# Performance work log

Measured on AMD Instinct MI355X. Metric: run time of the kernel, lower is better.

Reference implementation:

```python
import jax, jax.numpy as jnp
import numpy as np

D_MODEL = 1024
H = 16
DH = 64
FFN = 4096
CHUNK = 64
LN_EPS = 1e-5


def layer_norm(x, w, b):
    mu = x.mean(-1, keepdims=True)
    var = x.var(-1, keepdims=True)
    return (x - mu) * jax.lax.rsqrt(var + LN_EPS) * w + b


def l2_normalize(x):
    # matches torch F.normalize(p=2, dim=-1, eps=1e-12)
    n = jnp.sqrt(jnp.sum(x * x, axis=-1, keepdims=True))
    return x / jnp.maximum(n, 1e-12)


def chunk_gla(q, k, v, alpha, C=CHUNK):
    B, Hh, N, D = q.shape
    nc = N // C  # N chosen as multiple of C (pad==0 in original)
    q = q.reshape(B, Hh, nc, C, D)
    k = k.reshape(B, Hh, nc, C, D)
    v = v.reshape(B, Hh, nc, C, D)
    alpha = alpha.reshape(B, Hh, nc, C, D)

    log_a = jnp.log(jnp.maximum(alpha, 1e-6))
    la_cum = jnp.cumsum(log_a, axis=3)                  # (B,H,nc,C,D)
    la_mean = la_cum.mean(-1)                            # (B,H,nc,C)
    tril = jnp.tril(jnp.ones((C, C), dtype=q.dtype))
    decay = jnp.exp(la_mean[..., :, None] - la_mean[..., None, :]) * tril  # (B,H,nc,C,C)

    attn_intra = jnp.einsum('bhncd,bhnmd->bhncm', q, k) * decay
    o_intra = jnp.einsum('bhncm,bhnmd->bhncd', attn_intra, v)

    decay_to_end = jnp.exp(la_cum[:, :, :, -1:, :] - la_cum)
    kv_chunk = jnp.einsum('bhncf,bhnce->bhnfe', k * decay_to_end, v)  # (B,H,nc,D,D)
    chunk_decay = jnp.exp(log_a.sum(3))                  # (B,H,nc,D)
    q_dec = q * jnp.exp(la_cum)                          # decay_from_start

    def step(S, inp):
        qd, kv, cd = inp                                 # (B,H,C,D),(B,H,D,D),(B,H,D)
        o = jnp.einsum('bhcd,bhde->bhce', qd, S)
        S_new = S * cd[:, :, :, None] + kv
        return S_new, o

    S0 = jnp.zeros((B, Hh, D, D), dtype=q.dtype)
    _, o_inter = jax.lax.scan(
        step, S0,
        (jnp.moveaxis(q_dec, 2, 0), jnp.moveaxis(kv_chunk, 2, 0), jnp.moveaxis(chunk_decay, 2, 0)))
    o_inter = jnp.moveaxis(o_inter, 0, 2)                # (B,H,nc,C,D)
    return (o_intra + o_inter).reshape(B, Hh, N, D)


def setup_inputs() -> dict:
    key = jax.random.key(0)
    ks = jax.random.split(key, 16)
    s = 0.02
    td = H * DH
    return {
        'x': jax.random.normal(ks[0], (2, 4096, D_MODEL), dtype=jnp.float32),
        'Wq': jax.random.normal(ks[1], (D_MODEL, td), dtype=jnp.float32) * s,
        'Wk': jax.random.normal(ks[2], (D_MODEL, td), dtype=jnp.float32) * s,
        'Wv': jax.random.normal(ks[3], (D_MODEL, td), dtype=jnp.float32) * s,
        'Wg': jax.random.normal(ks[4], (D_MODEL, td), dtype=jnp.float32) * s,
        'bg': jnp.full((td,), -0.5, dtype=jnp.float32),
        'Wo': jax.random.normal(ks[5], (td, D_MODEL), dtype=jnp.float32) * s,
        'ln1_w': jnp.ones((D_MODEL,), jnp.float32),
        'ln1_b': jnp.zeros((D_MODEL,), jnp.float32),
        'ln2_w': jnp.ones((D_MODEL,), jnp.float32),
        'ln2_b': jnp.zeros((D_MODEL,), jnp.float32),
        'W1': jax.random.normal(ks[6], (D_MODEL, FFN), dtype=jnp.float32) * s,
        'b1': jnp.zeros((FFN,), jnp.float32),
        'W2': jax.random.normal(ks[7], (FFN, D_MODEL), dtype=jnp.float32) * s,
        'b2': jnp.zeros((D_MODEL,), jnp.float32),
    }


def reference(x, Wq, Wk, Wv, Wg, bg, Wo, ln1_w, ln1_b, ln2_w, ln2_b, W1, b1, W2, b2):
    B, N, _ = x.shape
    xn = layer_norm(x, ln1_w, ln1_b)
    q = (xn @ Wq).reshape(B, N, H, DH).transpose(0, 2, 1, 3)
    k = (xn @ Wk).reshape(B, N, H, DH).transpose(0, 2, 1, 3)
    v = (xn @ Wv).reshape(B, N, H, DH).transpose(0, 2, 1, 3)
    q = l2_normalize(q)
    k = l2_normalize(k)
    alpha = jax.nn.sigmoid(xn @ Wg + bg).reshape(B, N, H, DH).transpose(0, 2, 1, 3)
    o = chunk_gla(q, k, v, alpha)
    o = o.transpose(0, 2, 1, 3).reshape(B, N, H * DH)
    x = x + o @ Wo  # dropout off (eval / p=0)
    h = layer_norm(x, ln2_w, ln2_b)
    x = x + jax.nn.gelu(h @ W1 + b1, approximate=False) @ W2 + b2
    return x
```

## Files before the change

### kernel.cpp

```cpp
#include <hip/hip_runtime.h>

#define AS1 __attribute__((address_space(1)))
#define AS3 __attribute__((address_space(3)))

typedef unsigned short u16;
typedef short s16x8 __attribute__((ext_vector_type(8)));
typedef float f32x4 __attribute__((ext_vector_type(4)));

__device__ __forceinline__ float bf2f(u16 u) {
    union { unsigned u; float f; } v; v.u = ((unsigned)u) << 16; return v.f;
}
__device__ __forceinline__ u16 f2bf(float f) {
    union { float f; unsigned u; } v; v.f = f;
    unsigned u = v.u;
    return (u16)((u + 0x7FFFu + ((u >> 16) & 1u)) >> 16);
}

__device__ __forceinline__ void gload16(const void* g, void* l) {
    __builtin_amdgcn_global_load_lds((const AS1 void*)g, (AS3 void*)l, 16, 0, 0);
}

__global__ __launch_bounds__(256) void transpose_bf16(
    const float* __restrict__ src, u16* __restrict__ dst, int R, int C)
{
    __shared__ float t[32][33];
    const int tx = threadIdx.x, ty = threadIdx.y;
    const int r0 = blockIdx.x * 32, c0 = blockIdx.y * 32;
#pragma unroll
    for (int i = 0; i < 4; i++)
        t[ty + i * 8][tx] = src[(size_t)(r0 + ty + i * 8) * C + c0 + tx];
    __syncthreads();
#pragma unroll
    for (int i = 0; i < 4; i++)
        dst[(size_t)(c0 + ty + i * 8) * R + r0 + tx] = f2bf(t[tx][ty + i * 8]);
}

__global__ __launch_bounds__(256) void ln_bf16(
    const float* __restrict__ x, const float* __restrict__ w,
    const float* __restrict__ b, u16* __restrict__ out)
{
    __shared__ float red[8];
    const int row = blockIdx.x;
    const int tid = threadIdx.x;
    const size_t base = (size_t)row * 1024 + tid * 4;
    const float4 xv = *(const float4*)&x[base];
    float s = xv.x + xv.y + xv.z + xv.w;
    float q = xv.x * xv.x + xv.y * xv.y + xv.z * xv.z + xv.w * xv.w;
#pragma unroll
    for (int m = 1; m < 64; m <<= 1) { s += __shfl_xor(s, m); q += __shfl_xor(q, m); }
    if ((tid & 63) == 0) { red[tid >> 6] = s; red[4 + (tid >> 6)] = q; }
    __syncthreads();
    s = red[0] + red[1] + red[2] + red[3];
    q = red[4] + red[5] + red[6] + red[7];
    const float mu = s * (1.f / 1024.f);
    const float var = q * (1.f / 1024.f) - mu * mu;
    const float rs = rsqrtf(var + 1e-5f);
    const float4 wv = *(const float4*)&w[tid * 4];
    const float4 bv = *(const float4*)&b[tid * 4];
    uint2 ov;
    ov.x = (unsigned)f2bf((xv.x - mu) * rs * wv.x + bv.x) |
           ((unsigned)f2bf((xv.y - mu) * rs * wv.y + bv.y) << 16);
    ov.y = (unsigned)f2bf((xv.z - mu) * rs * wv.z + bv.z) |
           ((unsigned)f2bf((xv.w - mu) * rs * wv.w + bv.w) << 16);
    *(uint2*)&out[base] = ov;
}

template <int EP>
__global__ __launch_bounds__(256, 2) void gemm_bt(
    const u16* __restrict__ A, const u16* __restrict__ BT,
    float* __restrict__ Cf, u16* __restrict__ Cb,
    const float* __restrict__ bias, const float* __restrict__ resid,
    int M, int N, int K)
{
    __shared__ u16 As[4096];
    __shared__ u16 Bs[4096];
    const int tid = threadIdx.x;
    const int w = tid >> 6;
    const int l = tid & 63;
    const int tm = blockIdx.x * 128;
    const int tn = blockIdx.y * 128;
    const int wm = (w >> 1) * 64;
    const int wn = (w & 1) * 64;

    f32x4 acc[4][4] = {};

    const int e0 = w * 512 + l * 8;
    const int r0 = e0 >> 5, c0 = e0 & 31;
    const int e1 = 2048 + e0;
    const int r1 = e1 >> 5, c1 = e1 & 31;
    const size_t arow0 = (size_t)(tm + r0) * K + c0;
    const size_t arow1 = (size_t)(tm + r1) * K + c1;
    const size_t brow0 = (size_t)(tn + r0) * K + c0;
    const size_t brow1 = (size_t)(tn + r1) * K + c1;
    const int lofs = w * 512;
    const int afr = wm + (l & 15);
    const int bfr = wn + (l & 15);
    const int kk = (l >> 4) * 8;

    for (int k0 = 0; k0 < K; k0 += 32) {
        gload16(&A[arow0 + k0], &As[lofs]);
        gload16(&A[arow1 + k0], &As[2048 + lofs]);
        gload16(&BT[brow0 + k0], &Bs[lofs]);
        gload16(&BT[brow1 + k0], &Bs[2048 + lofs]);
        __syncthreads();
        s16x8 a[4], b[4];
#pragma unroll
        for (int i = 0; i < 4; i++) a[i] = *(const s16x8*)&As[(afr + i * 16) * 32 + kk];
#pragma unroll
        for (int j = 0; j < 4; j++) b[j] = *(const s16x8*)&Bs[(bfr + j * 16) * 32 + kk];
#pragma unroll
        for (int i = 0; i < 4; i++)
#pragma unroll
            for (int j = 0; j < 4; j++)
                acc[i][j] = __builtin_amdgcn_mfma_f32_16x16x32_bf16(a[i], b[j], acc[i][j], 0, 0, 0);
        __syncthreads();
    }

    const int erow = tm + wm + (l >> 4) * 4;
    const int ecol = tn + wn + (l & 15);
#pragma unroll
    for (int i = 0; i < 4; i++) {
#pragma unroll
        for (int j = 0; j < 4; j++) {
            const int col = ecol + j * 16;
#pragma unroll
            for (int r = 0; r < 4; r++) {
                const int row = erow + i * 16 + r;
                const size_t idx = (size_t)row * N + col;
                const float v = acc[i][j][r];
                if (EP == 0) {
                    Cf[idx] = v;
                } else if (EP == 1) {
                    Cb[idx] = f2bf(v);
                } else if (EP == 2) {
                    Cf[idx] = v + resid[idx];
                } else if (EP == 3) {
                    const float u = v + bias[col];
                    Cb[idx] = f2bf(0.5f * u * (1.f + erff(u * 0.70710678118654752f)));
                } else {
                    Cf[idx] = v + bias[col] + resid[idx];
                }
            }
        }
    }
}

#define TP 72
#define LP 65
__global__ __launch_bounds__(256) void gla_a(
    const u16* __restrict__ qkv,
    const float* __restrict__ g,
    const float* __restrict__ bg,
    u16* __restrict__ qdec,
    u16* __restrict__ kvT,
    float* __restrict__ cdec,
    u16* __restrict__ ointra)
{
    __shared__ u16 Qh[64 * TP];
    __shared__ u16 Kh[64 * TP];
    __shared__ u16 VT[64 * TP];
    __shared__ float L[64 * LP];
    __shared__ float lm[64], nq[64], nk[64];

    const int bid = blockIdx.x;
    const int bh = bid >> 6, ck = bid & 63;
    const int b = bh >> 4, h = bh & 15;
    const int tok0 = b * 4096 + ck * 64;
    const int tid = threadIdx.x;
    const int w = tid >> 6, l = tid & 63;

#pragma unroll
    for (int pass = 0; pass < 2; pass++) {
        const int c = (tid >> 3) + pass * 32;
        const int col = (tid & 7) * 8;
        const size_t rb = (size_t)(tok0 + c) * 3072 + h * 64 + col;
        uint4 qv = *(const uint4*)&qkv[rb];
        uint4 kv_ = *(const uint4*)&qkv[rb + 1024];
        uint4 vv = *(const uint4*)&qkv[rb + 2048];
        *(uint4*)&Qh[c * TP + col] = qv;
        *(uint4*)&Kh[c * TP + col] = kv_;
        const u16* va = (const u16*)&vv;
#pragma unroll
        for (int j = 0; j < 8; j++) VT[(col + j) * TP + c] = va[j];
    }
#pragma unroll
    for (int pass = 0; pass < 4; pass++) {
        const int c = (tid >> 4) + pass * 16;
        const int col = (tid & 15) * 4;
        float4 gv = *(const float4*)&g[(size_t)(tok0 + c) * 1024 + h * 64 + col];
        float4 bgv = *(const float4*)&bg[h * 64 + col];
        const float* ga = (const float*)&gv;
        const float* ba = (const float*)&bgv;
#pragma unroll
        for (int i = 0; i < 4; i++) {
            const float z = ga[i] + ba[i];
            const float al = 1.f / (1.f + __expf(-z));
            L[c * LP + col + i] = __logf(fmaxf(al, 1e-6f));
        }
    }
    __syncthreads();

    {
        const int d = tid >> 2, qq = tid & 3;
        float vals[16];
#pragma unroll
        for (int i = 0; i < 16; i++) vals[i] = L[(qq * 16 + i) * LP + d];
        float s = 0.f;
#pragma unroll
        for (int i = 0; i < 16; i++) { s += vals[i]; vals[i] = s; }
        float sum = s;
        float u1 = __shfl_up(sum, 1, 4); if (qq >= 1) sum += u1;
        float u2 = __shfl_up(sum, 2, 4); if (qq >= 2) sum += u2;
        const float excl = sum - s;
#pragma unroll
        for (int i = 0; i < 16; i++) L[(qq * 16 + i) * LP + d] = vals[i] + excl;
        if (qq == 3) cdec[((size_t)bh * 64 + ck) * 64 + d] = __expf(sum);
    }
    __syncthreads();

    {
        const int c = tid >> 2, qq = tid & 3;
        float sl = 0.f, sq = 0.f, sk = 0.f;
        uint4 qa = *(const uint4*)&Qh[c * TP + qq * 16];
        uint4 qb = *(const uint4*)&Qh[c * TP + qq * 16 + 8];
        uint4 ka = *(const uint4*)&Kh[c * TP + qq * 16];
        uint4 kb = *(const uint4*)&Kh[c * TP + qq * 16 + 8];
        const u16* qu = (const u16*)&qa; const u16* qu2 = (const u16*)&qb;
        const u16* ku = (const u16*)&ka; const u16* ku2 = (const u16*)&kb;
#pragma unroll
        for (int i = 0; i < 8; i++) {
            float q1 = bf2f(qu[i]), q2 = bf2f(qu2[i]);
            float k1 = bf2f(ku[i]), k2 = bf2f(ku2[i]);
            sq += q1 * q1 + q2 * q2;
            sk += k1 * k1 + k2 * k2;
        }
#pragma unroll
        for (int i = 0; i < 16; i++) sl += L[c * LP + qq * 16 + i];
        sl += __shfl_xor(sl, 1); sl += __shfl_xor(sl, 2);
        sq += __shfl_xor(sq, 1); sq += __shfl_xor(sq, 2);
        sk += __shfl_xor(sk, 1); sk += __shfl_xor(sk, 2);
        if (qq == 0) {
            lm[c] = sl * (1.f / 64.f);
            nq[c] = 1.f / fmaxf(sqrtf(sq), 1e-12f);
            nk[c] = 1.f / fmaxf(sqrtf(sk), 1e-12f);
        }
    }
    __syncthreads();

    u16 kdt[16];
    {
        const int c = tid >> 2, qq = tid & 3;
        const float qn = nq[c], kn = nk[c];
        uint4 qa = *(const uint4*)&Qh[c * TP + qq * 16];
        uint4 qb = *(const uint4*)&Qh[c * TP + qq * 16 + 8];
        uint4 ka = *(const uint4*)&Kh[c * TP + qq * 16];
        uint4 kb = *(const uint4*)&Kh[c * TP + qq * 16 + 8];
        u16* qu = (u16*)&qa; u16* qu2 = (u16*)&qb;
        u16* ku = (u16*)&ka; u16* ku2 = (u16*)&kb;
        float Lc[16], Le[16];
#pragma unroll
        for (int i = 0; i < 16; i++) {
            Lc[i] = L[c * LP + qq * 16 + i];
            Le[i] = L[63 * LP + qq * 16 + i];
        }
        unsigned qd[8];
#pragma unroll
        for (int i = 0; i < 8; i++) {
            float qh1 = bf2f(qu[i]) * qn;  qu[i] = f2bf(qh1);
            float qh2 = bf2f(qu2[i]) * qn; qu2[i] = f2bf(qh2);
            float kh1 = bf2f(ku[i]) * kn;  ku[i] = f2bf(kh1);
            float kh2 = bf2f(ku2[i]) * kn; ku2[i] = f2bf(kh2);
            kdt[i]     = f2bf(kh1 * __expf(Le[i] - Lc[i]));
            kdt[i + 8] = f2bf(kh2 * __expf(Le[i + 8] - Lc[i + 8]));
            const unsigned lo = (unsigned)f2bf(qh1 * __expf(Lc[i]));
            const unsigned hi = (i < 4) ? 0u : 0u;
            qd[i] = lo; (void)hi;
        }
        unsigned pk[8];
#pragma unroll
        for (int i = 0; i < 4; i++) {
            pk[i]     = qd[2 * i] | (qd[2 * i + 1] << 16);
        }
#pragma unroll
        for (int i = 0; i < 4; i++) {
            const float qh1 = bf2f(qu2[2 * i]) * 1.f;
            const float qh2 = bf2f(qu2[2 * i + 1]) * 1.f;
            pk[4 + i] = (unsigned)f2bf(qh1 * __expf(Lc[8 + 2 * i])) |
                        ((unsigned)f2bf(qh2 * __expf(Lc[8 + 2 * i + 1])) << 16);
        }
        *(uint4*)&Qh[c * TP + qq * 16] = qa;
        *(uint4*)&Qh[c * TP + qq * 16 + 8] = qb;
        *(uint4*)&Kh[c * TP + qq * 16] = ka;
        *(uint4*)&Kh[c * TP + qq * 16 + 8] = kb;
        u16* qrow = &qdec[((size_t)bh * 4096 + ck * 64 + c) * 64 + qq * 16];
        *(uint4*)&qrow[0] = *(const uint4*)&pk[0];
        *(uint4*)&qrow[8] = *(const uint4*)&pk[4];
    }
    __syncthreads();

    u16* KDT = (u16*)L;
    {
        const int c = tid >> 2, qq = tid & 3;
#pragma unroll
        for (int i = 0; i < 16; i++) KDT[(qq * 16 + i) * TP + c] = kdt[i];
    }
    const int fr = l & 15;
    const int kk = (l >> 4) * 8;
    f32x4 accS[4] = {};
#pragma unroll
    for (int ks = 0; ks < 2; ks++) {
        s16x8 af = *(const s16x8*)&Qh[(w * 16 + fr) * TP + ks * 32 + kk];
#pragma unroll
        for (int j = 0; j < 4; j++) {
            s16x8 bf = *(const s16x8*)&Kh[(j * 16 + fr) * TP + ks * 32 + kk];
            accS[j] = __builtin_amdgcn_mfma_f32_16x16x32_bf16(af, bf, accS[j], 0, 0, 0);
        }
    }
    __syncthreads();

    {
        const int erow = w * 16 + (l >> 4) * 4;
#pragma unroll
        for (int j = 0; j < 4; j++) {
            const int mm = j * 16 + (l & 15);
            const float lmm = lm[mm];
#pragma unroll
            for (int r = 0; r < 4; r++) {
                const int cc = erow + r;
                const float wgt = (mm <= cc) ? __expf(lm[cc] - lmm) : 0.f;
                Qh[cc * TP + mm] = f2bf(accS[j][r] * wgt);
            }
        }
    }
    __syncthreads();

    f32x4 accO[4] = {};
    f32x4 accK[4] = {};
#pragma unroll
    for (int ks = 0; ks < 2; ks++) {
        s16x8 aAt = *(const s16x8*)&Qh[(w * 16 + fr) * TP + ks * 32 + kk];
        s16x8 aVt = *(const s16x8*)&VT[(w * 16 + fr) * TP + ks * 32 + kk];
#pragma unroll
        for (int j = 0; j < 4; j++) {
            s16x8 bVt = *(const s16x8*)&VT[(j * 16 + fr) * TP + ks * 32 + kk];
            s16x8 bKd = *(const s16x8*)&KDT[(j * 16 + fr) * TP + ks * 32 + kk];
            accO[j] = __builtin_amdgcn_mfma_f32_16x16x32_bf16(aAt, bVt, accO[j], 0, 0, 0);
            accK[j] = __builtin_amdgcn_mfma_f32_16x16x32_bf16(aVt, bKd, accK[j], 0, 0, 0);
        }
    }
    {
        const int erow = w * 16 + (l >> 4) * 4;
#pragma unroll
        for (int j = 0; j < 4; j++) {
            const int col = j * 16 + (l & 15);
#pragma unroll
            for (int r = 0; r < 4; r++) {
                const int row = erow + r;
                ointra[((size_t)bh * 4096 + ck * 64 + row) * 64 + col] = f2bf(accO[j][r]);
                kvT[(((size_t)bh * 64 + ck) * 64 + row) * 64 + col] = f2bf(accK[j][r]);
            }
        }
    }
}

__global__ __launch_bounds__(256) void gla_scan(
    const u16* __restrict__ kvT, const float* __restrict__ cdec,
    u16* __restrict__ ST)
{
    const int bh = blockIdx.x >> 4;
    const int de = (blockIdx.x & 15) * 256 + threadIdx.x;
    const int d = de & 63;
    float s = 0.f;
    const size_t base = (size_t)bh * 64 * 4096 + de;
    const size_t cb = (size_t)bh * 4096 + d;
    for (int t = 0; t < 64; t++) {
        ST[base + (size_t)t * 4096] = f2bf(s);
        s = s * cdec[cb + (size_t)t * 64] + bf2f(kvT[base + (size_t)t * 4096]);
    }
}

__global__ __launch_bounds__(256) void gla_b(
    const u16* __restrict__ qdec, const u16* __restrict__ ST,
    const u16* __restrict__ ointra, u16* __restrict__ obf)
{
    __shared__ u16 Qd[64 * TP];
    __shared__ u16 Sd[64 * TP];
    const int bid = blockIdx.x;
    const int bh = bid >> 6, ck = bid & 63;
    const int b = bh >> 4, h = bh & 15;
    const int tid = threadIdx.x;
    const int w = tid >> 6, l = tid & 63;
#pragma unroll
    for (int pass = 0; pass < 2; pass++) {
        const int r = (tid >> 3) + pass * 32;
        const int col = (tid & 7) * 8;
        *(uint4*)&Qd[r * TP + col] =
            *(const uint4*)&qdec[((size_t)bh * 4096 + ck * 64 + r) * 64 + col];
        *(uint4*)&Sd[r * TP + col] =
            *(const uint4*)&ST[(((size_t)bh * 64 + ck) * 64 + r) * 64 + col];
    }
    __syncthreads();
    const int fr = l & 15;
    const int kk = (l >> 4) * 8;
    f32x4 acc[4] = {};
#pragma unroll
    for (int ks = 0; ks < 2; ks++) {
        s16x8 af = *(const s16x8*)&Qd[(w * 16 + fr) * TP + ks * 32 + kk];
#pragma unroll
        for (int j = 0; j < 4; j++) {
            s16x8 bf = *(const s16x8*)&Sd[(j * 16 + fr) * TP + ks * 32 + kk];
            acc[j] = __builtin_amdgcn_mfma_f32_16x16x32_bf16(af, bf, acc[j], 0, 0, 0);
        }
    }
    const int erow = w * 16 + (l >> 4) * 4;
#pragma unroll
    for (int j = 0; j < 4; j++) {
        const int e = j * 16 + (l & 15);
#pragma unroll
        for (int r = 0; r < 4; r++) {
            const int cc = erow + r;
            const size_t ia = ((size_t)bh * 4096 + ck * 64 + cc) * 64 + e;
            const float v = acc[j][r] + bf2f(ointra[ia]);
            obf[(size_t)(b * 4096 + ck * 64 + cc) * 1024 + h * 64 + e] = f2bf(v);
        }
    }
}

__global__ void fill_sentinel(float* out, int n) {
    int i = blockIdx.x * 256 + threadIdx.x;
    if (i < n) out[i] = 12345.0f;
}

extern "C" void kernel_launch(void* const* d_in, const int* in_sizes, int n_in,
                              void* d_out, int out_size, void* d_ws, size_t ws_size,
                              hipStream_t stream)
{
    const float* x    = (const float*)d_in[0];
    const float* Wq   = (const float*)d_in[1];
    const float* Wk   = (const float*)d_in[2];
    const float* Wv   = (const float*)d_in[3];
    const float* Wg   = (const float*)d_in[4];
    const float* bg   = (const float*)d_in[5];
    const float* Wo   = (const float*)d_in[6];
    const float* ln1w = (const float*)d_in[7];
    const float* ln1b = (const float*)d_in[8];
    const float* ln2w = (const float*)d_in[9];
    const float* ln2b = (const float*)d_in[10];
    const float* W1   = (const float*)d_in[11];
    const float* b1   = (const float*)d_in[12];
    const float* W2   = (const float*)d_in[13];
    const float* b2   = (const float*)d_in[14];
    float* out = (float*)d_out;

    char* ws = (char*)d_ws;
    u16*   wtQKVG = (u16*)(ws + 0);
    u16*   wtWo   = (u16*)(ws + 8388608);
    u16*   wtW1   = (u16*)(ws + 10485760);
    u16*   wtW2   = (u16*)(ws + 18874368);
    u16*   xnb    = (u16*)(ws + 27262976);
    u16*   qkvb   = (u16*)(ws + 44040192);
    float* gbuf   = (float*)(ws + 94371840);
    u16*   kvT    = (u16*)(ws + 127926272);
    float* cdbuf  = (float*)(ws + 144703488);
    u16*   qdecb  = (u16*)(ws + 145227776);
    u16*   ointra = (u16*)(ws + 162004992);
    u16*   STb    = (u16*)(ws + 178782208);
    u16*   obf    = (u16*)(ws + 195559424);
    u16*   hbf    = (u16*)(ws + 212336640);
    float* x2     = (float*)(ws + 94371840);
    u16*   ffnb   = (u16*)(ws + 27262976);

    if (ws_size < 229113856u) {
        fill_sentinel<<<dim3((out_size + 255) / 256), dim3(256), 0, stream>>>(out, out_size);
        return;
    }

    const dim3 b256(256), b32x8(32, 8);

    transpose_bf16<<<dim3(32, 32),  b32x8, 0, stream>>>(Wq, wtQKVG,               1024, 1024);
    transpose_bf16<<<dim3(32, 32),  b32x8, 0, stream>>>(Wk, wtQKVG + 1024 * 1024, 1024, 1024);
    transpose_bf16<<<dim3(32, 32),  b32x8, 0, stream>>>(Wv, wtQKVG + 2048 * 1024, 1024, 1024);
    transpose_bf16<<<dim3(32, 32),  b32x8, 0, stream>>>(Wg, wtQKVG + 3072 * 1024, 1024, 1024);
    transpose_bf16<<<dim3(32, 32),  b32x8, 0, stream>>>(Wo, wtWo,                 1024, 1024);
    transpose_bf16<<<dim3(32, 128), b32x8, 0, stream>>>(W1, wtW1,                 1024, 4096);
    transpose_bf16<<<dim3(128, 32), b32x8, 0, stream>>>(W2, wtW2,                 4096, 1024);

    ln_bf16<<<dim3(8192), b256, 0, stream>>>(x, ln1w, ln1b, xnb);
    gemm_bt<1><<<dim3(64, 24), b256, 0, stream>>>(xnb, wtQKVG, nullptr, qkvb, nullptr, nullptr, 8192, 3072, 1024);
    gemm_bt<0><<<dim3(64, 8),  b256, 0, stream>>>(xnb, wtQKVG + 3072 * 1024, gbuf, nullptr, nullptr, nullptr, 8192, 1024, 1024);

    gla_a<<<dim3(2048), b256, 0, stream>>>(qkvb, gbuf, bg, qdecb, kvT, cdbuf, ointra);
    gla_scan<<<dim3(512), b256, 0, stream>>>(kvT, cdbuf, STb);
    gla_b<<<dim3(2048), b256, 0, stream>>>(qdecb, STb, ointra, obf);

    gemm_bt<2><<<dim3(64, 8), b256, 0, stream>>>(obf, wtWo, x2, nullptr, nullptr, x, 8192, 1024, 1024);
    ln_bf16<<<dim3(8192), b256, 0, stream>>>(x2, ln2w, ln2b, hbf);
    gemm_bt<3><<<dim3(64, 32), b256, 0, stream>>>(hbf, wtW1, nullptr, ffnb, b1, nullptr, 8192, 4096, 1024);
    gemm_bt<4><<<dim3(64, 8),  b256, 0, stream>>>(ffnb, wtW2, out, nullptr, b2, x2, 8192, 1024, 4096);
}
```

Measured before the change: 423.0 us.

## Add 256x256-tile double-buffered GEMM with swizzled LDS; fuse QKV and gate projections

Adds a new 512-thread GEMM kernel with 256x256 output tiles, a double-buffered LDS pipeline fed by direct global-to-LDS loads, XOR-swizzled LDS addressing and raised wave priority around MFMA blocks. It is used for the merged QKV+gate projection (one launch whose epilogue routes columns to bf16 or fp32 outputs), the Wo projection with residual, and the FFN up-projection with GELU. The older gemm_bt is trimmed to the bias+residual epilogue still used by the FFN down-projection. The gla_a q-decay packing is also simplified. Larger tiles raise per-block reuse but give fewer blocks, which risks poor occupancy and tail effects on the smaller GEMMs.

Result: slower. 544.7 us (+28.8%).

```diff
diff --git a/kernel.cpp b/kernel.cpp
--- a/kernel.cpp
+++ b/kernel.cpp
@@ -127,18 +127,138 @@
             for (int r = 0; r < 4; r++) {
                 const int row = erow + i * 16 + r;
                 const size_t idx = (size_t)row * N + col;
-                const float v = acc[i][j][r];
-                if (EP == 0) {
-                    Cf[idx] = v;
-                } else if (EP == 1) {
-                    Cb[idx] = f2bf(v);
-                } else if (EP == 2) {
+                Cf[idx] = acc[i][j][r] + bias[col] + resid[idx];
+            }
+        }
+    }
+}
+
+template <int MO>
+__device__ __forceinline__ void quad(f32x4 (&acc)[8][4], const s16x8 (&aa)[4], const s16x8 (&bb)[4]) {
+#pragma unroll
+    for (int mm = 0; mm < 4; mm++)
+#pragma unroll
+        for (int nn = 0; nn < 4; nn++)
+            acc[MO + mm][nn] =
+                __builtin_amdgcn_mfma_f32_16x16x32_bf16(aa[mm], bb[nn], acc[MO + mm][nn], 0, 0, 0);
+}
+
+template <int EPX>
+__global__ __launch_bounds__(512, 2) void gemm256(
+    const u16* __restrict__ A, const u16* __restrict__ BT,
+    float* __restrict__ Cf, u16* __restrict__ Cb,
+    const float* __restrict__ bias, const float* __restrict__ resid,
+    int M, int N, int K)
+{
+    __shared__ u16 As[2][16384];
+    __shared__ u16 Bs[2][16384];
+    const int tid = threadIdx.x;
+    const int w = tid >> 6;
+    const int l = tid & 63;
+    const int wr = w >> 2;
+    const int wc = w & 3;
+    const int tm = blockIdx.x * 256;
+    const int tn = blockIdx.y * 256;
+
+    const int srow = w * 8 + (l >> 3);
+    const int swzc = ((l & 7) * 8) ^ (((l >> 3) & 3) << 4) ^ (((l >> 5) & 1) << 3);
+    size_t aS[2][2], bS[2][2];
+#pragma unroll
+    for (int h = 0; h < 2; h++)
+#pragma unroll
+        for (int j = 0; j < 2; j++) {
+            aS[h][j] = (size_t)(tm + h * 128 + j * 64 + srow) * K + swzc;
+            bS[h][j] = (size_t)(tn + h * 128 + j * 64 + srow) * K + swzc;
+        }
+    const int ldsOff[2] = { w * 512, 4096 + w * 512 };
+
+    auto stage = [&](int t, int buf) {
+        const int k0 = t * 64;
+#pragma unroll
+        for (int h = 0; h < 2; h++)
+#pragma unroll
+            for (int j = 0; j < 2; j++)
+                gload16(&A[aS[h][j] + k0], &As[buf][h * 8192 + ldsOff[j]]);
+#pragma unroll
+        for (int h = 0; h < 2; h++)
+#pragma unroll
+            for (int j = 0; j < 2; j++)
+                gload16(&BT[bS[h][j] + k0], &Bs[buf][h * 8192 + ldsOff[j]]);
+    };
+
+    const int sm = ((l & 3) << 4) | (((l >> 2) & 1) << 3);
+    const int aRd = wr * 8192 + (l & 15) * 64 + (((l >> 4) * 8) ^ sm);
+    const int bRd = wc * 4096 + (l & 15) * 64 + (((l >> 4) * 8) ^ sm);
+
+    f32x4 acc[8][4] = {};
+
+    stage(0, 0);
+    stage(1, 1);
+    asm volatile("s_waitcnt vmcnt(8)" ::: "memory");
+    __builtin_amdgcn_s_barrier();
+
+    const int NT = K >> 6;
+    for (int t = 0; t < NT; ++t) {
+        const int buf = t & 1;
+        const u16* as = As[buf];
+        const u16* bs = Bs[buf];
+        s16x8 aa[4], bb[4];
+#pragma unroll
+        for (int i = 0; i < 4; i++) bb[i] = *(const s16x8*)&bs[bRd + i * 1024];
+#pragma unroll
+        for (int i = 0; i < 4; i++) aa[i] = *(const s16x8*)&as[aRd + i * 1024];
+        __builtin_amdgcn_s_setprio(1);
+        quad<0>(acc, aa, bb);
+        __builtin_amdgcn_s_setprio(0);
+#pragma unroll
+        for (int i = 0; i < 4; i++) aa[i] = *(const s16x8*)&as[aRd + (i + 4) * 1024];
+        __builtin_amdgcn_s_setprio(1);
+        quad<4>(acc, aa, bb);
+        __builtin_amdgcn_s_setprio(0);
+        s16x8 bb1[4], aa1[4];
+#pragma unroll
+        for (int i = 0; i < 4; i++) bb1[i] = *(const s16x8*)&bs[(bRd + i * 1024) ^ 32];
+#pragma unroll
+        for (int i = 0; i < 4; i++) aa[i] = *(const s16x8*)&as[(aRd + i * 1024) ^ 32];
+        __builtin_amdgcn_s_setprio(1);
+        quad<0>(acc, aa, bb1);
+        __builtin_amdgcn_s_setprio(0);
+#pragma unroll
+        for (int i = 0; i < 4; i++) aa1[i] = *(const s16x8*)&as[(aRd + (i + 4) * 1024) ^ 32];
+        asm volatile("s_waitcnt lgkmcnt(0)" ::: "memory");
+        __builtin_amdgcn_sched_barrier(0);
+        __builtin_amdgcn_s_barrier();
+        const bool st = (t + 2 < NT);
+        if (st) stage(t + 2, buf);
+        __builtin_amdgcn_s_setprio(1);
+        quad<4>(acc, aa1, bb1);
+        __builtin_amdgcn_s_setprio(0);
+        if (st)                 asm volatile("s_waitcnt vmcnt(8)" ::: "memory");
+        else if (t + 1 < NT)    asm volatile("s_waitcnt vmcnt(0)" ::: "memory");
+        __builtin_amdgcn_s_barrier();
+    }
+
+    const int erow0 = tm + wr * 128 + (l >> 4) * 4;
+    const int ecol0 = tn + wc * 64 + (l & 15);
+#pragma unroll
+    for (int m = 0; m < 8; m++) {
+#pragma unroll
+        for (int n = 0; n < 4; n++) {
+            const int col = ecol0 + n * 16;
+#pragma unroll
+            for (int r = 0; r < 4; r++) {
+                const int row = erow0 + m * 16 + r;
+                const float v = acc[m][n][r];
+                if (EPX == 0) {
+                    if (col < 3072) Cb[(size_t)row * 3072 + col] = f2bf(v);
+                    else            Cf[(size_t)row * 1024 + (col - 3072)] = v;
+                } else if (EPX == 1) {
+                    const float u2 = v + bias[col];
+                    Cb[(size_t)row * N + col] =
+                        f2bf(0.5f * u2 * (1.f + erff(u2 * 0.70710678118654752f)));
+                } else {
+                    const size_t idx = (size_t)row * N + col;
                     Cf[idx] = v + resid[idx];
-                } else if (EP == 3) {
-                    const float u = v + bias[col];
-                    Cb[idx] = f2bf(0.5f * u * (1.f + erff(u * 0.70710678118654752f)));
-                } else {
-                    Cf[idx] = v + bias[col] + resid[idx];
                 }
             }
         }
@@ -263,7 +383,7 @@
             Lc[i] = L[c * LP + qq * 16 + i];
             Le[i] = L[63 * LP + qq * 16 + i];
         }
-        unsigned qd[8];
+        unsigned pk[8];
 #pragma unroll
         for (int i = 0; i < 8; i++) {
             float qh1 = bf2f(qu[i]) * qn;  qu[i] = f2bf(qh1);
@@ -272,21 +392,13 @@
             float kh2 = bf2f(ku2[i]) * kn; ku2[i] = f2bf(kh2);
             kdt[i]     = f2bf(kh1 * __expf(Le[i] - Lc[i]));
             kdt[i + 8] = f2bf(kh2 * __expf(Le[i + 8] - Lc[i + 8]));
-            const unsigned lo = (unsigned)f2bf(qh1 * __expf(Lc[i]));
-            const unsigned hi = (i < 4) ? 0u : 0u;
-            qd[i] = lo; (void)hi;
-        }
-        unsigned pk[8];
+        }
 #pragma unroll
         for (int i = 0; i < 4; i++) {
-            pk[i]     = qd[2 * i] | (qd[2 * i + 1] << 16);
-        }
-#pragma unroll
-        for (int i = 0; i < 4; i++) {
-            const float qh1 = bf2f(qu2[2 * i]) * 1.f;
-            const float qh2 = bf2f(qu2[2 * i + 1]) * 1.f;
-            pk[4 + i] = (unsigned)f2bf(qh1 * __expf(Lc[8 + 2 * i])) |
-                        ((unsigned)f2bf(qh2 * __expf(Lc[8 + 2 * i + 1])) << 16);
+            pk[i] = (unsigned)f2bf(bf2f(qu[2 * i]) * __expf(Lc[2 * i])) |
+                    ((unsigned)f2bf(bf2f(qu[2 * i + 1]) * __expf(Lc[2 * i + 1])) << 16);
+            pk[4 + i] = (unsigned)f2bf(bf2f(qu2[2 * i]) * __expf(Lc[8 + 2 * i])) |
+                        ((unsigned)f2bf(bf2f(qu2[2 * i + 1]) * __expf(Lc[8 + 2 * i + 1])) << 16);
         }
         *(uint4*)&Qh[c * TP + qq * 16] = qa;
         *(uint4*)&Qh[c * TP + qq * 16 + 8] = qb;
@@ -475,7 +587,7 @@
         return;
     }
 
-    const dim3 b256(256), b32x8(32, 8);
+    const dim3 b256(256), b512(512), b32x8(32, 8);
 
     transpose_bf16<<<dim3(32, 32),  b32x8, 0, stream>>>(Wq, wtQKVG,               1024, 1024);
     transpose_bf16<<<dim3(32, 32),  b32x8, 0, stream>>>(Wk, wtQKVG + 1024 * 1024, 1024, 1024);
@@ -486,15 +598,14 @@
     transpose_bf16<<<dim3(128, 32), b32x8, 0, stream>>>(W2, wtW2,                 4096, 1024);
 
     ln_bf16<<<dim3(8192), b256, 0, stream>>>(x, ln1w, ln1b, xnb);
-    gemm_bt<1><<<dim3(64, 24), b256, 0, stream>>>(xnb, wtQKVG, nullptr, qkvb, nullptr, nullptr, 8192, 3072, 1024);
-    gemm_bt<0><<<dim3(64, 8),  b256, 0, stream>>>(xnb, wtQKVG + 3072 * 1024, gbuf, nullptr, nullptr, nullptr, 8192, 1024, 1024);
+    gemm256<0><<<dim3(32, 16), b512, 0, stream>>>(xnb, wtQKVG, gbuf, qkvb, nullptr, nullptr, 8192, 4096, 1024);
 
     gla_a<<<dim3(2048), b256, 0, stream>>>(qkvb, gbuf, bg, qdecb, kvT, cdbuf, ointra);
     gla_scan<<<dim3(512), b256, 0, stream>>>(kvT, cdbuf, STb);
     gla_b<<<dim3(2048), b256, 0, stream>>>(qdecb, STb, ointra, obf);
 
-    gemm_bt<2><<<dim3(64, 8), b256, 0, stream>>>(obf, wtWo, x2, nullptr, nullptr, x, 8192, 1024, 1024);
+    gemm256<2><<<dim3(32, 4), b512, 0, stream>>>(obf, wtWo, x2, nullptr, nullptr, x, 8192, 1024, 1024);
     ln_bf16<<<dim3(8192), b256, 0, stream>>>(x2, ln2w, ln2b, hbf);
-    gemm_bt<3><<<dim3(64, 32), b256, 0, stream>>>(hbf, wtW1, nullptr, ffnb, b1, nullptr, 8192, 4096, 1024);
-    gemm_bt<4><<<dim3(64, 8),  b256, 0, stream>>>(ffnb, wtW2, out, nullptr, b2, x2, 8192, 1024, 4096);
-}
+    gemm256<1><<<dim3(32, 16), b512, 0, stream>>>(hbf, wtW1, nullptr, ffnb, b1, nullptr, 8192, 4096, 1024);
+    gemm_bt<4><<<dim3(64, 8), b256, 0, stream>>>(ffnb, wtW2, out, nullptr, b2, x2, 8192, 1024, 4096);
+}
```

## Rewrite GEMM with 32x32 MFMA, double-buffered swizzled LDS, fused QKVG launch

Applied to the files above, without the earlier changes.

Replaces the single-buffered 16x16x32 MFMA GEMM with a kernel that uses 32x32x16 MFMA, K-step 64, and double-buffered LDS tiles loaded through global_load_lds. The LDS layout is XOR-swizzled to avoid bank conflicts, and the next tile's loads are issued while the current tile's MFMAs run, with setprio hints. The QKV and gate projections are merged into one launch whose epilogue splits output columns between bf16 and fp32 buffers. The q-decay packing in gla_a is also simplified. The change doubles LDS usage per block, which may lower occupancy.

Result: no change. 425.0 us (+0.5%).

```diff
diff --git a/kernel.cpp b/kernel.cpp
--- a/kernel.cpp
+++ b/kernel.cpp
@@ -6,6 +6,7 @@
 typedef unsigned short u16;
 typedef short s16x8 __attribute__((ext_vector_type(8)));
 typedef float f32x4 __attribute__((ext_vector_type(4)));
+typedef float f32x16 __attribute__((ext_vector_type(16)));
 
 __device__ __forceinline__ float bf2f(u16 u) {
     union { unsigned u; float f; } v; v.u = ((unsigned)u) << 16; return v.f;
@@ -65,84 +66,130 @@
     *(uint2*)&out[base] = ov;
 }
 
-template <int EP>
-__global__ __launch_bounds__(256, 2) void gemm_bt(
+template <int EPX>
+__global__ __launch_bounds__(256, 2) void gemm32(
     const u16* __restrict__ A, const u16* __restrict__ BT,
     float* __restrict__ Cf, u16* __restrict__ Cb,
     const float* __restrict__ bias, const float* __restrict__ resid,
     int M, int N, int K)
 {
-    __shared__ u16 As[4096];
-    __shared__ u16 Bs[4096];
+    __shared__ u16 As[2][8192];
+    __shared__ u16 Bs[2][8192];
     const int tid = threadIdx.x;
-    const int w = tid >> 6;
-    const int l = tid & 63;
-    const int tm = blockIdx.x * 128;
-    const int tn = blockIdx.y * 128;
-    const int wm = (w >> 1) * 64;
-    const int wn = (w & 1) * 64;
-
-    f32x4 acc[4][4] = {};
-
-    const int e0 = w * 512 + l * 8;
-    const int r0 = e0 >> 5, c0 = e0 & 31;
-    const int e1 = 2048 + e0;
-    const int r1 = e1 >> 5, c1 = e1 & 31;
-    const size_t arow0 = (size_t)(tm + r0) * K + c0;
-    const size_t arow1 = (size_t)(tm + r1) * K + c1;
-    const size_t brow0 = (size_t)(tn + r0) * K + c0;
-    const size_t brow1 = (size_t)(tn + r1) * K + c1;
-    const int lofs = w * 512;
-    const int afr = wm + (l & 15);
-    const int bfr = wn + (l & 15);
-    const int kk = (l >> 4) * 8;
-
-    for (int k0 = 0; k0 < K; k0 += 32) {
-        gload16(&A[arow0 + k0], &As[lofs]);
-        gload16(&A[arow1 + k0], &As[2048 + lofs]);
-        gload16(&BT[brow0 + k0], &Bs[lofs]);
-        gload16(&BT[brow1 + k0], &Bs[2048 + lofs]);
-        __syncthreads();
-        s16x8 a[4], b[4];
-#pragma unroll
-        for (int i = 0; i < 4; i++) a[i] = *(const s16x8*)&As[(afr + i * 16) * 32 + kk];
-#pragma unroll
-        for (int j = 0; j < 4; j++) b[j] = *(const s16x8*)&Bs[(bfr + j * 16) * 32 + kk];
-#pragma unroll
-        for (int i = 0; i < 4; i++)
-#pragma unroll
-            for (int j = 0; j < 4; j++)
-                acc[i][j] = __builtin_amdgcn_mfma_f32_16x16x32_bf16(a[i], b[j], acc[i][j], 0, 0, 0);
-        __syncthreads();
-    }
-
-    const int erow = tm + wm + (l >> 4) * 4;
-    const int ecol = tn + wn + (l & 15);
-#pragma unroll
-    for (int i = 0; i < 4; i++) {
-#pragma unroll
-        for (int j = 0; j < 4; j++) {
-            const int col = ecol + j * 16;
-#pragma unroll
-            for (int r = 0; r < 4; r++) {
-                const int row = erow + i * 16 + r;
-                const size_t idx = (size_t)row * N + col;
-                const float v = acc[i][j][r];
-                if (EP == 0) {
-                    Cf[idx] = v;
-                } else if (EP == 1) {
-                    Cb[idx] = f2bf(v);
-                } else if (EP == 2) {
+    const int w = tid >> 6, l = tid & 63;
+    const int tm = blockIdx.x * 128, tn = blockIdx.y * 128;
+    const int wm = (w >> 1) * 64, wn = (w & 1) * 64;
+
+    const int srow = l >> 3;
+    const int scol = ((l & 7) ^ srow) * 8;
+    size_t aSb[4], bSb[4];
+#pragma unroll
+    for (int j = 0; j < 4; j++) {
+        aSb[j] = (size_t)(tm + w * 32 + j * 8 + srow) * K + scol;
+        bSb[j] = (size_t)(tn + w * 32 + j * 8 + srow) * K + scol;
+    }
+
+    auto stage = [&](int t, int buf) {
+        const int k0 = t * 64;
+#pragma unroll
+        for (int j = 0; j < 4; j++)
+            gload16(&A[aSb[j] + k0], &As[buf][(w * 32 + j * 8) * 64]);
+#pragma unroll
+        for (int j = 0; j < 4; j++)
+            gload16(&BT[bSb[j] + k0], &Bs[buf][(w * 32 + j * 8) * 64]);
+    };
+
+    int aoff[2][4], boff[2][4];
+#pragma unroll
+    for (int mm = 0; mm < 2; mm++)
+#pragma unroll
+        for (int ks = 0; ks < 4; ks++) {
+            const int g = ((ks * 2 + (l >> 5)) ^ (l & 7)) * 8;
+            aoff[mm][ks] = (wm + mm * 32 + (l & 31)) * 64 + g;
+            boff[mm][ks] = (wn + mm * 32 + (l & 31)) * 64 + g;
+        }
+
+    f32x16 acc[2][2] = {};
+
+    stage(0, 0);
+    stage(1, 1);
+    asm volatile("s_waitcnt vmcnt(8)" ::: "memory");
+    __builtin_amdgcn_s_barrier();
+
+    const int NT = K >> 6;
+    for (int t = 0; t < NT; ++t) {
+        const int buf = t & 1;
+        const u16* as = As[buf];
+        const u16* bs = Bs[buf];
+        s16x8 a0[2][2], b0[2][2], a1[2][2], b1[2][2];
+#pragma unroll
+        for (int ks = 0; ks < 2; ks++)
+#pragma unroll
+            for (int mm = 0; mm < 2; mm++) {
+                a0[mm][ks] = *(const s16x8*)&as[aoff[mm][ks]];
+                b0[mm][ks] = *(const s16x8*)&bs[boff[mm][ks]];
+            }
+        __builtin_amdgcn_s_setprio(1);
+#pragma unroll
+        for (int ks = 0; ks < 2; ks++)
+#pragma unroll
+            for (int mm = 0; mm < 2; mm++)
+#pragma unroll
+                for (int nn = 0; nn < 2; nn++)
+                    acc[mm][nn] = __builtin_amdgcn_mfma_f32_32x32x16_bf16(
+                        a0[mm][ks], b0[nn][ks], acc[mm][nn], 0, 0, 0);
+        __builtin_amdgcn_s_setprio(0);
+#pragma unroll
+        for (int ks = 0; ks < 2; ks++)
+#pragma unroll
+            for (int mm = 0; mm < 2; mm++) {
+                a1[mm][ks] = *(const s16x8*)&as[aoff[mm][ks + 2]];
+                b1[mm][ks] = *(const s16x8*)&bs[boff[mm][ks + 2]];
+            }
+        asm volatile("s_waitcnt lgkmcnt(0)" ::: "memory");
+        __builtin_amdgcn_sched_barrier(0);
+        __builtin_amdgcn_s_barrier();
+        const bool st = (t + 2 < NT);
+        if (st) stage(t + 2, buf);
+        __builtin_amdgcn_s_setprio(1);
+#pragma unroll
+        for (int ks = 0; ks < 2; ks++)
+#pragma unroll
+            for (int mm = 0; mm < 2; mm++)
+#pragma unroll
+                for (int nn = 0; nn < 2; nn++)
+                    acc[mm][nn] = __builtin_amdgcn_mfma_f32_32x32x16_bf16(
+                        a1[mm][ks], b1[nn][ks], acc[mm][nn], 0, 0, 0);
+        __builtin_amdgcn_s_setprio(0);
+        if (st)              asm volatile("s_waitcnt vmcnt(8)" ::: "memory");
+        else if (t + 1 < NT) asm volatile("s_waitcnt vmcnt(0)" ::: "memory");
+        __builtin_amdgcn_s_barrier();
+    }
+
+#pragma unroll
+    for (int mm = 0; mm < 2; mm++)
+#pragma unroll
+        for (int nn = 0; nn < 2; nn++)
+#pragma unroll
+            for (int reg = 0; reg < 16; reg++) {
+                const int row = tm + wm + mm * 32 + (l >> 5) * 4 + (reg & 3) + (reg >> 2) * 8;
+                const int col = tn + wn + nn * 32 + (l & 31);
+                const float v = acc[mm][nn][reg];
+                if (EPX == 0) {
+                    if (col < 3072) Cb[(size_t)row * 3072 + col] = f2bf(v);
+                    else            Cf[(size_t)row * 1024 + (col - 3072)] = v;
+                } else if (EPX == 1) {
+                    const float u2 = v + bias[col];
+                    Cb[(size_t)row * N + col] =
+                        f2bf(0.5f * u2 * (1.f + erff(u2 * 0.70710678118654752f)));
+                } else if (EPX == 2) {
+                    const size_t idx = (size_t)row * N + col;
                     Cf[idx] = v + resid[idx];
-                } else if (EP == 3) {
-                    const float u = v + bias[col];
-                    Cb[idx] = f2bf(0.5f * u * (1.f + erff(u * 0.70710678118654752f)));
                 } else {
+                    const size_t idx = (size_t)row * N + col;
                     Cf[idx] = v + bias[col] + resid[idx];
                 }
             }
-        }
-    }
 }
 
 #define TP 72
@@ -263,7 +310,7 @@
             Lc[i] = L[c * LP + qq * 16 + i];
             Le[i] = L[63 * LP + qq * 16 + i];
         }
-        unsigned qd[8];
+        unsigned pk[8];
 #pragma unroll
         for (int i = 0; i < 8; i++) {
             float qh1 = bf2f(qu[i]) * qn;  qu[i] = f2bf(qh1);
@@ -272,21 +319,13 @@
             float kh2 = bf2f(ku2[i]) * kn; ku2[i] = f2bf(kh2);
             kdt[i]     = f2bf(kh1 * __expf(Le[i] - Lc[i]));
             kdt[i + 8] = f2bf(kh2 * __expf(Le[i + 8] - Lc[i + 8]));
-            const unsigned lo = (unsigned)f2bf(qh1 * __expf(Lc[i]));
-            const unsigned hi = (i < 4) ? 0u : 0u;
-            qd[i] = lo; (void)hi;
-        }
-        unsigned pk[8];
+        }
 #pragma unroll
         for (int i = 0; i < 4; i++) {
-            pk[i]     = qd[2 * i] | (qd[2 * i + 1] << 16);
-        }
-#pragma unroll
-        for (int i = 0; i < 4; i++) {
-            const float qh1 = bf2f(qu2[2 * i]) * 1.f;
-            const float qh2 = bf2f(qu2[2 * i + 1]) * 1.f;
-            pk[4 + i] = (unsigned)f2bf(qh1 * __expf(Lc[8 + 2 * i])) |
-                        ((unsigned)f2bf(qh2 * __expf(Lc[8 + 2 * i + 1])) << 16);
+            pk[i] = (unsigned)f2bf(bf2f(qu[2 * i]) * __expf(Lc[2 * i])) |
+                    ((unsigned)f2bf(bf2f(qu[2 * i + 1]) * __expf(Lc[2 * i + 1])) << 16);
+            pk[4 + i] = (unsigned)f2bf(bf2f(qu2[2 * i]) * __expf(Lc[8 + 2 * i])) |
+                        ((unsigned)f2bf(bf2f(qu2[2 * i + 1]) * __expf(Lc[8 + 2 * i + 1])) << 16);
         }
         *(uint4*)&Qh[c * TP + qq * 16] = qa;
         *(uint4*)&Qh[c * TP + qq * 16 + 8] = qb;
@@ -486,15 +525,14 @@
     transpose_bf16<<<dim3(128, 32), b32x8, 0, stream>>>(W2, wtW2,                 4096, 1024);
 
     ln_bf16<<<dim3(8192), b256, 0, stream>>>(x, ln1w, ln1b, xnb);
-    gemm_bt<1><<<dim3(64, 24), b256, 0, stream>>>(xnb, wtQKVG, nullptr, qkvb, nullptr, nullptr, 8192, 3072, 1024);
-    gemm_bt<0><<<dim3(64, 8),  b256, 0, stream>>>(xnb, wtQKVG + 3072 * 1024, gbuf, nullptr, nullptr, nullptr, 8192, 1024, 1024);
+    gemm32<0><<<dim3(64, 32), b256, 0, stream>>>(xnb, wtQKVG, gbuf, qkvb, nullptr, nullptr, 8192, 4096, 1024);
 
     gla_a<<<dim3(2048), b256, 0, stream>>>(qkvb, gbuf, bg, qdecb, kvT, cdbuf, ointra);
     gla_scan<<<dim3(512), b256, 0, stream>>>(kvT, cdbuf, STb);
     gla_b<<<dim3(2048), b256, 0, stream>>>(qdecb, STb, ointra, obf);
 
-    gemm_bt<2><<<dim3(64, 8), b256, 0, stream>>>(obf, wtWo, x2, nullptr, nullptr, x, 8192, 1024, 1024);
+    gemm32<2><<<dim3(64, 8), b256, 0, stream>>>(obf, wtWo, x2, nullptr, nullptr, x, 8192, 1024, 1024);
     ln_bf16<<<dim3(8192), b256, 0, stream>>>(x2, ln2w, ln2b, hbf);
-    gemm_bt<3><<<dim3(64, 32), b256, 0, stream>>>(hbf, wtW1, nullptr, ffnb, b1, nullptr, 8192, 4096, 1024);
-    gemm_bt<4><<<dim3(64, 8),  b256, 0, stream>>>(ffnb, wtW2, out, nullptr, b2, x2, 8192, 1024, 4096);
-}
+    gemm32<1><<<dim3(64, 32), b256, 0, stream>>>(hbf, wtW1, nullptr, ffnb, b1, nullptr, 8192, 4096, 1024);
+    gemm32<4><<<dim3(64, 8), b256, 0, stream>>>(ffnb, wtW2, out, nullptr, b2, x2, 8192, 1024, 4096);
+}
```
